# Kernel optimization log

Measured on AMD Instinct MI355X. Metric: run time of the kernel, lower is better.

## Reference

```python
import jax, jax.numpy as jnp
import numpy as np

S_DIM, T_DIM, FEAT_DIM = 2048, 2048, 128
NCE_N, NCE_T, NCE_MOM = 16384, 0.07, 0.5
N_DATA, BATCH = 100000, 64
EPS = 1e-7


def _l2norm(x):
    return x / jnp.linalg.norm(x, axis=1, keepdims=True)


def setup_inputs() -> dict:
    key = jax.random.key(0)
    ks = jax.random.split(key, 10)
    feat_s = jax.random.normal(ks[0], (BATCH, S_DIM), dtype=jnp.float32)
    feat_t = jax.random.normal(ks[1], (BATCH, T_DIM), dtype=jnp.float32)
    idx = jax.random.randint(ks[2], (BATCH,), 0, N_DATA)
    sample_idx = jax.random.randint(ks[3], (BATCH, NCE_N + 1), 0, N_DATA)
    sample_idx = sample_idx.at[:, 0].set(idx)  # positive sample in column 0
    # Embed linear weights (Linear(dim_in, feat_dim))
    w_s = jax.random.normal(ks[4], (FEAT_DIM, S_DIM), dtype=jnp.float32) / np.sqrt(S_DIM)
    b_s = jnp.zeros((FEAT_DIM,), dtype=jnp.float32)
    w_t = jax.random.normal(ks[5], (FEAT_DIM, T_DIM), dtype=jnp.float32) / np.sqrt(T_DIM)
    b_t = jnp.zeros((FEAT_DIM,), dtype=jnp.float32)
    # memory banks, uniform(-stdv, stdv), stdv = 1/sqrt(feat_dim/3)
    stdv = 1.0 / np.sqrt(FEAT_DIM / 3.0)
    mem_v1 = jax.random.uniform(ks[6], (N_DATA, FEAT_DIM), dtype=jnp.float32, minval=-stdv, maxval=stdv)
    mem_v2 = jax.random.uniform(ks[7], (N_DATA, FEAT_DIM), dtype=jnp.float32, minval=-stdv, maxval=stdv)
    return {"feat_s": feat_s, "feat_t": feat_t, "idx": idx, "sample_idx": sample_idx,
            "w_s": w_s, "b_s": b_s, "w_t": w_t, "b_t": b_t,
            "mem_v1": mem_v1, "mem_v2": mem_v2}


def _contrast_out(mem, samp_idx, v):
    # gather [B, K+1, D] from memory bank, bmm against [B, D]
    w = mem[samp_idx]                                # [B, K+1, D]
    logits = jnp.einsum('bkd,bd->bk', w, v) / NCE_T  # [B, K+1]
    out = jnp.exp(logits)
    z = jnp.mean(out) * N_DATA                       # first-pass Z estimate
    return out / z


def _contrast_loss(x):
    b = x.shape[0]
    m = float(NCE_N) / N_DATA
    log_d1 = jnp.log(x[:, 0] / (x[:, 0] + m + EPS))          # positives
    log_d0 = jnp.log(m / (x[:, 1:] + m + EPS))               # negatives
    return -(jnp.sum(log_d1) + jnp.sum(log_d0)) / b


def reference(feat_s, feat_t, idx, sample_idx, w_s, b_s, w_t, b_t, mem_v1, mem_v2):
    hs = _l2norm(feat_s @ w_s.T + b_s)  # [B, D]
    ht = _l2norm(feat_t @ w_t.T + b_t)  # [B, D]
    out_s = _contrast_out(mem_v2, sample_idx, hs)  # anchor=student vs teacher memory
    out_t = _contrast_out(mem_v1, sample_idx, ht)  # anchor=teacher vs student memory
    return _contrast_loss(out_s) + _contrast_loss(out_t)
```

## Files before the change

### kernel.cpp

```cpp
#include <hip/hip_runtime.h>

#define DIM_IN   2048
#define FEAT     128
#define KP1      16385
#define NDATA    100000
#define BATCH    64
#define NBG      32
#define NTG      (NDATA / NBG)
#define GCH      32
#define LCH      8

constexpr float NCE_T_INV = 1.0f / 0.07f;
constexpr float M_CONST   = 16384.0f / 100000.0f;
constexpr float EPS_C     = 1e-7f;

typedef short bf16x8 __attribute__((ext_vector_type(8)));
typedef float f32x4  __attribute__((ext_vector_type(4)));

#define VP_PLANE 34816
#define VP_SIDE  17408
#define VP_ROW   272

__global__ void __launch_bounds__(1024) embed_kernel(
    const float* __restrict__ feat_s, const float* __restrict__ feat_t,
    const float* __restrict__ w_s, const float* __restrict__ b_s,
    const float* __restrict__ w_t, const float* __restrict__ b_t,
    char* __restrict__ vplanes, float* __restrict__ z_zero,
    float* __restrict__ out_zero)
{
    const int blk  = blockIdx.x;
    const int side = blk >> 6;
    const int b    = blk & 63;
    const float* feat = (side == 0 ? feat_s : feat_t) + (size_t)b * DIM_IN;
    const float* w    = (side == 0 ? w_s : w_t);
    const float* bias = (side == 0 ? b_s : b_t);

    __shared__ float sfeat[DIM_IN];
    __shared__ float pre[FEAT];
    __shared__ float wsum[2];

    const int t = threadIdx.x;
    if (blk == 0) {
        if (t < 128) z_zero[t] = 0.f;
        else if (t == 128) out_zero[0] = 0.f;
    }
    {
        const float4* f4 = (const float4*)feat;
        float4* s4 = (float4*)sfeat;
        if (t < 512) s4[t] = f4[t];
    }
    __syncthreads();

    const int wv = t >> 6, ln = t & 63;
    const float4* w4  = (const float4*)w;
    const float4* sf4 = (const float4*)sfeat;
#pragma unroll 2
    for (int i = 0; i < 8; ++i) {
        const int d = wv + i * 16;
        float s = 0.f;
#pragma unroll
        for (int seg = 0; seg < 8; ++seg) {
            float4 a = w4[d * (DIM_IN / 4) + seg * 64 + ln];
            float4 f = sf4[seg * 64 + ln];
            s += a.x * f.x + a.y * f.y + a.z * f.z + a.w * f.w;
        }
#pragma unroll
        for (int o = 32; o > 0; o >>= 1) s += __shfl_xor(s, o, 64);
        if (ln == 0) pre[d] = s;
    }
    __syncthreads();

    if (t < 128) {
        float p = pre[t] + bias[t];
        pre[t] = p;
        float sq = p * p;
#pragma unroll
        for (int o = 32; o > 0; o >>= 1) sq += __shfl_xor(sq, o, 64);
        if ((t & 63) == 0) wsum[t >> 6] = sq;
    }
    __syncthreads();
    if (t < 128) {
        float inv_norm = 1.0f / sqrtf(wsum[0] + wsum[1]);
        float x = pre[t] * inv_norm;
        unsigned int u = __float_as_uint(x);
        unsigned short h = (unsigned short)(u >> 16);
        float hf = __uint_as_float(u & 0xffff0000u);
        float lr = x - hf;
        unsigned short l = (unsigned short)(__float_as_uint(lr) >> 16);
        const size_t off = (size_t)side * VP_SIDE + (size_t)b * VP_ROW + t * 2;
        *(unsigned short*)(vplanes + off)            = h;
        *(unsigned short*)(vplanes + VP_PLANE + off) = l;
    }
}

__global__ void __launch_bounds__(256) gemm_exp_kernel(
    const float* __restrict__ mem_v1, const float* __restrict__ mem_v2,
    const char* __restrict__ vplanes, float* __restrict__ E)
{
    __shared__ __align__(16) char lds[51200];

    const int bx   = blockIdx.x;
    const int side = bx & 1;
    const int tile = bx >> 1;
    const int n0   = tile * NBG;
    const float* bank = (side == 0 ? mem_v2 : mem_v1);
    const int t  = threadIdx.x;
    const int wv = t >> 6, ln = t & 63;
    const int lm = ln & 15;
    const int kb = ln >> 4;
    const int ntile = wv & 1;
    const int mpair = wv >> 1;
    const int nloc  = ntile * 16 + lm;

    {
        const char* bbase = (const char*)bank;
        for (int s = wv; s < 16; s += 4) {
            const int o   = s * 1024 + ln * 16;
            const int row = o >> 9;
            const int so  = (o & ~511) | ((o & 511) ^ ((row & 7) << 4));
            const size_t g = (size_t)n0 * 512 + so;
            __builtin_amdgcn_global_load_lds(
                (const __attribute__((address_space(1))) void*)(bbase + g),
                (__attribute__((address_space(3))) void*)(lds + 34816 + s * 1024),
                16, 0, 0);
        }
    }
    {
        const char* hbase = vplanes + (size_t)side * VP_SIDE;
        const char* lbase = vplanes + VP_PLANE + (size_t)side * VP_SIDE;
        for (int seg = wv; seg < 34; seg += 4) {
            const char* src = (seg < 17 ? hbase + seg * 1024
                                        : lbase + (seg - 17) * 1024) + ln * 16;
            __builtin_amdgcn_global_load_lds(
                (const __attribute__((address_space(1))) void*)src,
                (__attribute__((address_space(3))) void*)(lds + seg * 1024),
                16, 0, 0);
        }
    }

    f32x4 acc[2];
    acc[0] = (f32x4){0.f, 0.f, 0.f, 0.f};
    acc[1] = (f32x4){0.f, 0.f, 0.f, 0.f};

    __syncthreads();

    const int sw = (nloc & 7) << 4;
#pragma unroll
    for (int c = 0; c < 4; ++c) {
        const int bofs = nloc * 512 + c * 128 + kb * 32;
        const float4 f0 = *(const float4*)(lds + 34816 + ((bofs)      ^ sw));
        const float4 f1 = *(const float4*)(lds + 34816 + ((bofs + 16) ^ sw));
        const float xs[8] = {f0.x, f0.y, f0.z, f0.w, f1.x, f1.y, f1.z, f1.w};
        bf16x8 bh, bl;
#pragma unroll
        for (int j = 0; j < 8; ++j) {
            unsigned int u = __float_as_uint(xs[j]);
            bh[j] = (short)(u >> 16);
            float hf = __uint_as_float(u & 0xffff0000u);
            bl[j] = (short)(__float_as_uint(xs[j] - hf) >> 16);
        }
#pragma unroll
        for (int i = 0; i < 2; ++i) {
            const int mi = mpair * 2 + i;
            bf16x8 ah = *(const bf16x8*)(lds + (mi * 16 + lm) * VP_ROW + c * 64 + kb * 16);
            bf16x8 al = *(const bf16x8*)(lds + 17408 + (mi * 16 + lm) * VP_ROW + c * 64 + kb * 16);
            acc[i] = __builtin_amdgcn_mfma_f32_16x16x32_bf16(ah, bh, acc[i], 0, 0, 0);
            acc[i] = __builtin_amdgcn_mfma_f32_16x16x32_bf16(al, bh, acc[i], 0, 0, 0);
            acc[i] = __builtin_amdgcn_mfma_f32_16x16x32_bf16(ah, bl, acc[i], 0, 0, 0);
        }
    }

    const int nn = n0 + nloc;
    if (nn < NDATA) {
#pragma unroll
        for (int i = 0; i < 2; ++i) {
            const int mi = mpair * 2 + i;
#pragma unroll
            for (int jj = 0; jj < 4; ++jj) {
                const int anchor = mi * 16 + kb * 4 + jj;
                E[(size_t)(side * 64 + anchor) * NDATA + nn] =
                    __expf(acc[i][jj] * NCE_T_INV);
            }
        }
    }
}

__global__ void __launch_bounds__(256) gather_z_kernel(
    const int* __restrict__ sample_idx, const float* __restrict__ E,
    float* __restrict__ ex_out, float* __restrict__ z_out)
{
    const int blk   = blockIdx.x;
    const int chunk = blk >> 6;
    const int b     = blk & 63;
    const float* E0 = E + (size_t)b * NDATA;
    const float* E1 = E + (size_t)(64 + b) * NDATA;

    float zp0 = 0.f, zp1 = 0.f;
    for (int k = chunk * 256 + threadIdx.x; k < KP1; k += GCH * 256) {
        const int idx = sample_idx[(size_t)b * KP1 + k];
        const float e0 = E0[idx];
        const float e1 = E1[idx];
        ex_out[(size_t)b * KP1 + k]        = e0;
        ex_out[(size_t)(64 + b) * KP1 + k] = e1;
        zp0 += e0;
        zp1 += e1;
    }
#pragma unroll
    for (int o = 32; o > 0; o >>= 1) {
        zp0 += __shfl_xor(zp0, o, 64);
        zp1 += __shfl_xor(zp1, o, 64);
    }
    __shared__ float zw0[4], zw1[4];
    if ((threadIdx.x & 63) == 0) {
        zw0[threadIdx.x >> 6] = zp0;
        zw1[threadIdx.x >> 6] = zp1;
    }
    __syncthreads();
    if (threadIdx.x == 0) {
        atomicAdd(&z_out[b],      zw0[0] + zw0[1] + zw0[2] + zw0[3]);
        atomicAdd(&z_out[64 + b], zw1[0] + zw1[1] + zw1[2] + zw1[3]);
    }
}

__global__ void __launch_bounds__(256) loss_kernel(
    const float* __restrict__ ex_in, const float* __restrict__ z_in,
    float* __restrict__ out)
{
    const int blk   = blockIdx.x;
    const int chunk = blk >> 6;
    const int b     = blk & 63;

    __shared__ float zsh[2];
    if (threadIdx.x < 128) {
        float zv = z_in[threadIdx.x];
#pragma unroll
        for (int o = 32; o > 0; o >>= 1) zv += __shfl_xor(zv, o, 64);
        if ((threadIdx.x & 63) == 0) zsh[threadIdx.x >> 6] = zv;
    }
    __syncthreads();

    const float scale = (float)NDATA / (64.0f * (float)KP1);
    const float rz0 = 1.0f / (zsh[0] * scale);
    const float rz1 = 1.0f / (zsh[1] * scale);
    const float* ex0 = ex_in + (size_t)b * KP1;
    const float* ex1 = ex_in + (size_t)(64 + b) * KP1;

    float part = 0.f;
    for (int k = chunk * 256 + threadIdx.x; k < KP1; k += LCH * 256) {
        const float x0 = ex0[k] * rz0;
        const float x1 = ex1[k] * rz1;
        if (k == 0) {
            part += __logf(x0 / (x0 + M_CONST + EPS_C));
            part += __logf(x1 / (x1 + M_CONST + EPS_C));
        } else {
            part += __logf(M_CONST / (x0 + M_CONST + EPS_C));
            part += __logf(M_CONST / (x1 + M_CONST + EPS_C));
        }
    }
#pragma unroll
    for (int o = 32; o > 0; o >>= 1) part += __shfl_xor(part, o, 64);
    __shared__ float pw[4];
    if ((threadIdx.x & 63) == 0) pw[threadIdx.x >> 6] = part;
    __syncthreads();
    if (threadIdx.x == 0)
        atomicAdd(out, -(pw[0] + pw[1] + pw[2] + pw[3]) * (1.0f / 64.0f));
}

extern "C" void kernel_launch(void* const* d_in, const int* in_sizes, int n_in,
                              void* d_out, int out_size, void* d_ws, size_t ws_size,
                              hipStream_t stream)
{
    const float* feat_s     = (const float*)d_in[0];
    const float* feat_t     = (const float*)d_in[1];
    const int*   sample_idx = (const int*)  d_in[3];
    const float* w_s        = (const float*)d_in[4];
    const float* b_s        = (const float*)d_in[5];
    const float* w_t        = (const float*)d_in[6];
    const float* b_t        = (const float*)d_in[7];
    const float* mem_v1     = (const float*)d_in[8];
    const float* mem_v2     = (const float*)d_in[9];
    float* out = (float*)d_out;

    char*  ws     = (char*)d_ws;
    float* ws_z   = (float*)ws;
    float* ws_ex  = (float*)(ws + 512);
    char*  ws_vp  = (char*)(ws + 512);
    float* ws_E   = (float*)(ws + 512 + (size_t)2 * BATCH * KP1 * sizeof(float));

    embed_kernel<<<2 * BATCH, 1024, 0, stream>>>(feat_s, feat_t, w_s, b_s, w_t, b_t,
                                                 ws_vp, ws_z, out);
    gemm_exp_kernel<<<2 * NTG, 256, 0, stream>>>(mem_v1, mem_v2, ws_vp, ws_E);
    gather_z_kernel<<<BATCH * GCH, 256, 0, stream>>>(sample_idx, ws_E, ws_ex, ws_z);
    loss_kernel<<<BATCH * LCH, 256, 0, stream>>>(ws_ex, ws_z, out);
}
```

Baseline: 204.0 us.

## Make gemm_exp persistent over 8 tiles with double-buffered bank loads; vectorize gather/loss

```diff
diff --git a/kernel.cpp b/kernel.cpp
--- a/kernel.cpp
+++ b/kernel.cpp
@@ -6,9 +6,12 @@
 #define NDATA    100000
 #define BATCH    64
 #define NBG      32
-#define NTG      (NDATA / NBG)
-#define GCH      32
-#define LCH      8
+#define TPB      8
+#define RPB      (NBG * TPB)
+#define NBLK2    ((NDATA + RPB - 1) / RPB)
+#define GCH      8
+#define LCH      4
+#define EXR      16388
 
 constexpr float NCE_T_INV = 1.0f / 0.07f;
 constexpr float M_CONST   = 16384.0f / 100000.0f;
@@ -97,12 +100,11 @@
     const float* __restrict__ mem_v1, const float* __restrict__ mem_v2,
     const char* __restrict__ vplanes, float* __restrict__ E)
 {
-    __shared__ __align__(16) char lds[51200];
+    __shared__ __align__(16) char lds[67584];
 
     const int bx   = blockIdx.x;
     const int side = bx & 1;
-    const int tile = bx >> 1;
-    const int n0   = tile * NBG;
+    const int blk0 = (bx >> 1) * RPB;
     const float* bank = (side == 0 ? mem_v2 : mem_v1);
     const int t  = threadIdx.x;
     const int wv = t >> 6, ln = t & 63;
@@ -112,19 +114,9 @@
     const int mpair = wv >> 1;
     const int nloc  = ntile * 16 + lm;
 
-    {
-        const char* bbase = (const char*)bank;
-        for (int s = wv; s < 16; s += 4) {
-            const int o   = s * 1024 + ln * 16;
-            const int row = o >> 9;
-            const int so  = (o & ~511) | ((o & 511) ^ ((row & 7) << 4));
-            const size_t g = (size_t)n0 * 512 + so;
-            __builtin_amdgcn_global_load_lds(
-                (const __attribute__((address_space(1))) void*)(bbase + g),
-                (__attribute__((address_space(3))) void*)(lds + 34816 + s * 1024),
-                16, 0, 0);
-        }
-    }
+    const size_t bmax = (size_t)NDATA * 512 - 16;
+    const char* bbase = (const char*)bank;
+
     {
         const char* hbase = vplanes + (size_t)side * VP_SIDE;
         const char* lbase = vplanes + VP_PLANE + (size_t)side * VP_SIDE;
@@ -137,49 +129,86 @@
                 16, 0, 0);
         }
     }
-
-    f32x4 acc[2];
-    acc[0] = (f32x4){0.f, 0.f, 0.f, 0.f};
-    acc[1] = (f32x4){0.f, 0.f, 0.f, 0.f};
-
-    __syncthreads();
+#pragma unroll
+    for (int s0 = 0; s0 < 4; ++s0) {
+        const int s   = wv + s0 * 4;
+        const int o   = s * 1024 + ln * 16;
+        const int row = o >> 9;
+        const int so  = (o & ~511) | ((o & 511) ^ ((row & 7) << 4));
+        size_t g = (size_t)blk0 * 512 + so;
+        if (g > bmax) g = bmax;
+        __builtin_amdgcn_global_load_lds(
+            (const __attribute__((address_space(1))) void*)(bbase + g),
+            (__attribute__((address_space(3))) void*)(lds + 34816 + s * 1024),
+            16, 0, 0);
+    }
 
     const int sw = (nloc & 7) << 4;
-#pragma unroll
-    for (int c = 0; c < 4; ++c) {
-        const int bofs = nloc * 512 + c * 128 + kb * 32;
-        const float4 f0 = *(const float4*)(lds + 34816 + ((bofs)      ^ sw));
-        const float4 f1 = *(const float4*)(lds + 34816 + ((bofs + 16) ^ sw));
-        const float xs[8] = {f0.x, f0.y, f0.z, f0.w, f1.x, f1.y, f1.z, f1.w};
-        bf16x8 bh, bl;
-#pragma unroll
-        for (int j = 0; j < 8; ++j) {
-            unsigned int u = __float_as_uint(xs[j]);
-            bh[j] = (short)(u >> 16);
-            float hf = __uint_as_float(u & 0xffff0000u);
-            bl[j] = (short)(__float_as_uint(xs[j] - hf) >> 16);
-        }
-#pragma unroll
-        for (int i = 0; i < 2; ++i) {
-            const int mi = mpair * 2 + i;
-            bf16x8 ah = *(const bf16x8*)(lds + (mi * 16 + lm) * VP_ROW + c * 64 + kb * 16);
-            bf16x8 al = *(const bf16x8*)(lds + 17408 + (mi * 16 + lm) * VP_ROW + c * 64 + kb * 16);
-            acc[i] = __builtin_amdgcn_mfma_f32_16x16x32_bf16(ah, bh, acc[i], 0, 0, 0);
-            acc[i] = __builtin_amdgcn_mfma_f32_16x16x32_bf16(al, bh, acc[i], 0, 0, 0);
-            acc[i] = __builtin_amdgcn_mfma_f32_16x16x32_bf16(ah, bl, acc[i], 0, 0, 0);
-        }
-    }
-
-    const int nn = n0 + nloc;
-    if (nn < NDATA) {
-#pragma unroll
-        for (int i = 0; i < 2; ++i) {
-            const int mi = mpair * 2 + i;
-#pragma unroll
-            for (int jj = 0; jj < 4; ++jj) {
-                const int anchor = mi * 16 + kb * 4 + jj;
-                E[(size_t)(side * 64 + anchor) * NDATA + nn] =
-                    __expf(acc[i][jj] * NCE_T_INV);
+
+#pragma unroll 1
+    for (int tt = 0; tt < TPB; ++tt) {
+        if (tt == 0) asm volatile("s_waitcnt vmcnt(0)" ::: "memory");
+        else         asm volatile("s_waitcnt vmcnt(8)" ::: "memory");
+        __builtin_amdgcn_s_barrier();
+
+        if (tt + 1 < TPB) {
+            const int n1 = blk0 + (tt + 1) * NBG;
+            const int bb = ((tt + 1) & 1) * 16384;
+#pragma unroll
+            for (int s0 = 0; s0 < 4; ++s0) {
+                const int s   = wv + s0 * 4;
+                const int o   = s * 1024 + ln * 16;
+                const int row = o >> 9;
+                const int so  = (o & ~511) | ((o & 511) ^ ((row & 7) << 4));
+                size_t g = (size_t)n1 * 512 + so;
+                if (g > bmax) g = bmax;
+                __builtin_amdgcn_global_load_lds(
+                    (const __attribute__((address_space(1))) void*)(bbase + g),
+                    (__attribute__((address_space(3))) void*)(lds + 34816 + bb + s * 1024),
+                    16, 0, 0);
+            }
+        }
+
+        const char* B = lds + 34816 + (tt & 1) * 16384;
+        f32x4 acc[2];
+        acc[0] = (f32x4){0.f, 0.f, 0.f, 0.f};
+        acc[1] = (f32x4){0.f, 0.f, 0.f, 0.f};
+#pragma unroll
+        for (int c = 0; c < 4; ++c) {
+            const int bofs = nloc * 512 + c * 128 + kb * 32;
+            const float4 f0 = *(const float4*)(B + ((bofs)      ^ sw));
+            const float4 f1 = *(const float4*)(B + ((bofs + 16) ^ sw));
+            const float xs[8] = {f0.x, f0.y, f0.z, f0.w, f1.x, f1.y, f1.z, f1.w};
+            bf16x8 bh, bl;
+#pragma unroll
+            for (int j = 0; j < 8; ++j) {
+                unsigned int u = __float_as_uint(xs[j]);
+                bh[j] = (short)(u >> 16);
+                float hf = __uint_as_float(u & 0xffff0000u);
+                bl[j] = (short)(__float_as_uint(xs[j] - hf) >> 16);
+            }
+#pragma unroll
+            for (int i = 0; i < 2; ++i) {
+                const int mi = mpair * 2 + i;
+                bf16x8 ah = *(const bf16x8*)(lds + (mi * 16 + lm) * VP_ROW + c * 64 + kb * 16);
+                bf16x8 al = *(const bf16x8*)(lds + 17408 + (mi * 16 + lm) * VP_ROW + c * 64 + kb * 16);
+                acc[i] = __builtin_amdgcn_mfma_f32_16x16x32_bf16(ah, bh, acc[i], 0, 0, 0);
+                acc[i] = __builtin_amdgcn_mfma_f32_16x16x32_bf16(al, bh, acc[i], 0, 0, 0);
+                acc[i] = __builtin_amdgcn_mfma_f32_16x16x32_bf16(ah, bl, acc[i], 0, 0, 0);
+            }
+        }
+
+        const int nn = blk0 + tt * NBG + nloc;
+        if (nn < NDATA) {
+#pragma unroll
+            for (int i = 0; i < 2; ++i) {
+                const int mi = mpair * 2 + i;
+#pragma unroll
+                for (int jj = 0; jj < 4; ++jj) {
+                    const int anchor = mi * 16 + kb * 4 + jj;
+                    E[(size_t)(side * 64 + anchor) * NDATA + nn] =
+                        __expf(acc[i][jj] * NCE_T_INV);
+                }
             }
         }
     }
@@ -192,18 +221,30 @@
     const int blk   = blockIdx.x;
     const int chunk = blk >> 6;
     const int b     = blk & 63;
+    const int* sidx = sample_idx + (size_t)b * KP1;
     const float* E0 = E + (size_t)b * NDATA;
     const float* E1 = E + (size_t)(64 + b) * NDATA;
 
     float zp0 = 0.f, zp1 = 0.f;
-    for (int k = chunk * 256 + threadIdx.x; k < KP1; k += GCH * 256) {
-        const int idx = sample_idx[(size_t)b * KP1 + k];
-        const float e0 = E0[idx];
-        const float e1 = E1[idx];
-        ex_out[(size_t)b * KP1 + k]        = e0;
-        ex_out[(size_t)(64 + b) * KP1 + k] = e1;
-        zp0 += e0;
-        zp1 += e1;
+    for (int g = chunk * 256 + threadIdx.x; g < 4096; g += GCH * 256) {
+        const int i0 = sidx[g * 4 + 0];
+        const int i1 = sidx[g * 4 + 1];
+        const int i2 = sidx[g * 4 + 2];
+        const int i3 = sidx[g * 4 + 3];
+        float4 v0, v1;
+        v0.x = E0[i0]; v0.y = E0[i1]; v0.z = E0[i2]; v0.w = E0[i3];
+        v1.x = E1[i0]; v1.y = E1[i1]; v1.z = E1[i2]; v1.w = E1[i3];
+        *(float4*)&ex_out[(size_t)b * EXR + g * 4]        = v0;
+        *(float4*)&ex_out[(size_t)(64 + b) * EXR + g * 4] = v1;
+        zp0 += v0.x + v0.y + v0.z + v0.w;
+        zp1 += v1.x + v1.y + v1.z + v1.w;
+    }
+    if (chunk == 0 && threadIdx.x == 0) {
+        const int it = sidx[16384];
+        const float ta = E0[it], tb = E1[it];
+        ex_out[(size_t)b * EXR + 16384]        = ta;
+        ex_out[(size_t)(64 + b) * EXR + 16384] = tb;
+        zp0 += ta; zp1 += tb;
     }
 #pragma unroll
     for (int o = 32; o > 0; o >>= 1) {
@@ -242,19 +283,28 @@
     const float scale = (float)NDATA / (64.0f * (float)KP1);
     const float rz0 = 1.0f / (zsh[0] * scale);
     const float rz1 = 1.0f / (zsh[1] * scale);
-    const float* ex0 = ex_in + (size_t)b * KP1;
-    const float* ex1 = ex_in + (size_t)(64 + b) * KP1;
+    const float* ex0 = ex_in + (size_t)b * EXR;
+    const float* ex1 = ex_in + (size_t)(64 + b) * EXR;
 
     float part = 0.f;
-    for (int k = chunk * 256 + threadIdx.x; k < KP1; k += LCH * 256) {
-        const float x0 = ex0[k] * rz0;
-        const float x1 = ex1[k] * rz1;
-        if (k == 0) {
-            part += __logf(x0 / (x0 + M_CONST + EPS_C));
-            part += __logf(x1 / (x1 + M_CONST + EPS_C));
-        } else {
-            part += __logf(M_CONST / (x0 + M_CONST + EPS_C));
-            part += __logf(M_CONST / (x1 + M_CONST + EPS_C));
+    for (int g = chunk * 256 + threadIdx.x; g < 4097; g += LCH * 256) {
+        const float4 a0 = *(const float4*)&ex0[g * 4];
+        const float4 a1 = *(const float4*)&ex1[g * 4];
+        const float e0[4] = {a0.x, a0.y, a0.z, a0.w};
+        const float e1[4] = {a1.x, a1.y, a1.z, a1.w};
+#pragma unroll
+        for (int j = 0; j < 4; ++j) {
+            const int k = g * 4 + j;
+            if (k >= KP1) break;
+            const float x0 = e0[j] * rz0;
+            const float x1 = e1[j] * rz1;
+            if (k == 0) {
+                part += __logf(x0 / (x0 + M_CONST + EPS_C));
+                part += __logf(x1 / (x1 + M_CONST + EPS_C));
+            } else {
+                part += __logf(M_CONST / (x0 + M_CONST + EPS_C));
+                part += __logf(M_CONST / (x1 + M_CONST + EPS_C));
+            }
         }
     }
 #pragma unroll
@@ -285,11 +335,11 @@
     float* ws_z   = (float*)ws;
     float* ws_ex  = (float*)(ws + 512);
     char*  ws_vp  = (char*)(ws + 512);
-    float* ws_E   = (float*)(ws + 512 + (size_t)2 * BATCH * KP1 * sizeof(float));
+    float* ws_E   = (float*)(ws + 512 + (size_t)128 * EXR * sizeof(float));
 
     embed_kernel<<<2 * BATCH, 1024, 0, stream>>>(feat_s, feat_t, w_s, b_s, w_t, b_t,
                                                  ws_vp, ws_z, out);
-    gemm_exp_kernel<<<2 * NTG, 256, 0, stream>>>(mem_v1, mem_v2, ws_vp, ws_E);
+    gemm_exp_kernel<<<2 * NBLK2, 256, 0, stream>>>(mem_v1, mem_v2, ws_vp, ws_E);
     gather_z_kernel<<<BATCH * GCH, 256, 0, stream>>>(sample_idx, ws_E, ws_ex, ws_z);
     loss_kernel<<<BATCH * LCH, 256, 0, stream>>>(ws_ex, ws_z, out);
 }
```

After: 197.3 us. 1.03x faster.
